# Performance work log

Hardware: AMD Instinct MI355X
Metric: run time of the kernel (lower is better)

## Reference

```python
import jax, jax.numpy as jnp
import numpy as np

BN_EPS = 1e-5


def _gru(x, Wih, Whh, bih, bhh):
    # x: [B,S,D]; Wih: [3H,D]; Whh: [3H,H]; PyTorch gate order (r, z, n)
    B, S, D = x.shape
    H = Whh.shape[1]
    xg = jnp.einsum('bsd,gd->bsg', x, Wih) + bih  # [B,S,3H] precomputed input gates

    def step(h, xg_t):
        hg = h @ Whh.T + bhh
        xr, xz, xn = jnp.split(xg_t, 3, axis=-1)
        hr, hz, hn = jnp.split(hg, 3, axis=-1)
        r = jax.nn.sigmoid(xr + hr)
        z = jax.nn.sigmoid(xz + hz)
        n = jnp.tanh(xn + r * hn)
        h_new = (1.0 - z) * n + z * h
        return h_new, h_new

    h0 = jnp.zeros((B, H), x.dtype)
    _, hs = jax.lax.scan(step, h0, jnp.swapaxes(xg, 0, 1))  # [S,B,H]
    return jnp.swapaxes(hs, 0, 1)


def _lstm(x, Wih, Whh, bih, bhh):
    # x: [B,S,D]; PyTorch gate order (i, f, g, o)
    B, S, D = x.shape
    H = Whh.shape[1]
    xg = jnp.einsum('bsd,gd->bsg', x, Wih) + bih  # [B,S,4H]

    def step(carry, xg_t):
        h, c = carry
        g = xg_t + h @ Whh.T + bhh
        i, f, gg, o = jnp.split(g, 4, axis=-1)
        i = jax.nn.sigmoid(i)
        f = jax.nn.sigmoid(f)
        gg = jnp.tanh(gg)
        o = jax.nn.sigmoid(o)
        c_new = f * c + i * gg
        h_new = o * jnp.tanh(c_new)
        return (h_new, c_new), h_new

    h0 = jnp.zeros((B, H), x.dtype)
    c0 = jnp.zeros((B, H), x.dtype)
    _, hs = jax.lax.scan(step, (h0, c0), jnp.swapaxes(xg, 0, 1))
    return jnp.swapaxes(hs, 0, 1)


def setup_inputs() -> dict:
    key = jax.random.key(0)
    B, S, D, H = 64, 512, 40, 512
    ks = jax.random.split(key, 16)
    s_in = 1.0 / np.sqrt(H)

    def u(k, shape):
        return jax.random.uniform(k, shape, jnp.float32, -s_in, s_in)

    inp = {
        'x': jax.random.normal(ks[0], (B, S, D), jnp.float32),
        # rec1: GRU
        'gru_Wih': u(ks[1], (3 * H, D)),
        'gru_Whh': u(ks[2], (3 * H, H)),
        'gru_bih': u(ks[3], (3 * H,)),
        'gru_bhh': u(ks[4], (3 * H,)),
        # rec2: LSTM over [x, ssr] -> input D+1
        'lstm_Wih': u(ks[5], (4 * H, D + 1)),
        'lstm_Whh': u(ks[6], (4 * H, H)),
        'lstm_bih': u(ks[7], (4 * H,)),
        'lstm_bhh': u(ks[8], (4 * H,)),
        # fc1/fc2/fc3: hidden -> 1
        'fc1_w': u(ks[9], (1, H)), 'fc1_b': u(ks[10], (1,)),
        'fc2_w': u(ks[11], (1, H)), 'fc2_b': u(ks[12], (1,)),
        'fc3_w': u(ks[13], (1, H)), 'fc3_b': u(ks[14], (1,)),
        # BatchNorm1d affine params
        'bn_gamma': jnp.ones((H,), jnp.float32),
        'bn_beta': jnp.zeros((H,), jnp.float32),
    }
    return inp


def reference(x, gru_Wih, gru_Whh, gru_bih, gru_bhh,
              lstm_Wih, lstm_Whh, lstm_bih, lstm_bhh,
              fc1_w, fc1_b, fc2_w, fc2_b, fc3_w, fc3_b,
              bn_gamma, bn_beta):
    B, S, D = x.shape
    o1 = _gru(x, gru_Wih, gru_Whh, gru_bih, gru_bhh)  # [B,S,H]
    # BatchNorm1d (training mode): per-channel stats over (batch, time)
    mean = jnp.mean(o1, axis=(0, 1))
    var = jnp.mean((o1 - mean) ** 2, axis=(0, 1))
    o1 = (o1 - mean) * jax.lax.rsqrt(var + BN_EPS) * bn_gamma + bn_beta
    # gated scalar channel (dropout p=0 is identity)
    sr = jax.nn.relu(o1 @ fc1_w.T + fc1_b)            # [B,S,1]
    w = jnp.abs(jax.nn.sigmoid(o1 @ fc2_w.T + fc2_b))  # [B,S,1]
    ssr = sr * (w + 1.0)                              # [B,S,1]
    x2 = jnp.concatenate([x, ssr], axis=2)            # [B,S,D+1]
    o2 = _lstm(x2, lstm_Wih, lstm_Whh, lstm_bih, lstm_bhh)
    out = jax.nn.relu(o2 @ fc3_w.T + fc3_b)           # [B,S,1]
    return out, ssr
```

## Files before the change

### kernel.cpp

```cpp
#include <hip/hip_runtime.h>
#include <stdint.h>

#define GW 16
#define NU 32
#define HD 512
#define SEQ 512
#define DX 40
#define MB 16

using short8 = __attribute__((ext_vector_type(8))) short;
using f32x4  = __attribute__((ext_vector_type(4))) float;
typedef unsigned long long u64;

__device__ __forceinline__ unsigned short f2bf(float f) {
  uint32_t u = __builtin_bit_cast(uint32_t, f);
  u += 0x7fffu + ((u >> 16) & 1u);
  return (unsigned short)(u >> 16);
}
__device__ __forceinline__ float sigm(float x) { return 1.0f / (1.0f + __expf(-x)); }

#define MFMA_B16(a, b, c) __builtin_amdgcn_mfma_f32_16x16x32_bf16((a), (b), (c), 0, 0, 0)


__global__ __launch_bounds__(640, 1) void gru_kernel(
    const float* __restrict__ x, const float* __restrict__ Wih,
    const float* __restrict__ Whh, const float* __restrict__ bih,
    const float* __restrict__ bhh, unsigned* __restrict__ flags,
    u64* __restrict__ hbuf, float* __restrict__ o1, float* __restrict__ stats)
{
  const int wg = blockIdx.x & (GW - 1);
  const int g  = blockIdx.x >> 4;
  const int tid = threadIdx.x;
  const int wave = tid >> 6;
  const int lane = tid & 63;
  const int u0 = wg * NU;
  const int bg = g * MB;

  __shared__ __align__(16) unsigned short h_s[2][MB][520];
  __shared__ __align__(16) unsigned short x_s[2][MB][72];
  __shared__ float gate_s[3][MB][NU];
  __shared__ float xn_s[MB][NU];
  __shared__ uint32_t h_stage[256];
  __shared__ uint32_t sync_s[4];

  short8 bfrag[18];
  const int myGate = wave >> 1;
  const int ut = wave & 1;
  const int kq = (lane >> 4) * 8;
  if (wave < 6) {
    const int row = myGate * HD + u0 + ut * 16 + (lane & 15);
    for (int kt = 0; kt < 16; ++kt) {
      const float* p = Whh + (size_t)row * HD + kt * 32 + kq;
      short8 f;
#pragma unroll
      for (int j = 0; j < 8; ++j) f[j] = (short)f2bf(p[j]);
      bfrag[kt] = f;
    }
    for (int kt = 16; kt < 18; ++kt) {
      short8 f;
#pragma unroll
      for (int j = 0; j < 8; ++j) {
        int c = kt * 32 + kq + j - HD;
        float v = (myGate < 2 && c < DX) ? Wih[(size_t)row * DX + c] : 0.0f;
        f[j] = (short)f2bf(v);
      }
      bfrag[kt] = f;
    }
  } else if (wave < 8) {
    const int row = 2 * HD + u0 + (wave - 6) * 16 + (lane & 15);
    for (int kt = 0; kt < 2; ++kt) {
      short8 f;
#pragma unroll
      for (int j = 0; j < 8; ++j) {
        int c = kt * 32 + kq + j;
        f[j] = (short)((c < DX) ? f2bf(Wih[(size_t)row * DX + c]) : 0);
      }
      bfrag[kt] = f;
    }
  }

  const int sb = tid >> 5;
  const int su = tid & 31;
  float b_r = 0.f, b_z = 0.f, b_in = 0.f, b_hn = 0.f;
  if (tid < 256) {
    b_r  = bih[u0 + su] + bhh[u0 + su];
    b_z  = bih[HD + u0 + su] + bhh[HD + u0 + su];
    b_in = bih[2 * HD + u0 + su];
    b_hn = bhh[2 * HD + u0 + su];
  }

  for (int i = tid; i < 4160; i += 640) ((u64*)h_s)[i] = 0ull;
  for (int i = tid; i < 576;  i += 640) ((u64*)x_s)[i] = 0ull;
  if (tid < 4) sync_s[tid] = 0;
  __syncthreads();
  {
    int r = tid / 40, c = tid % 40;
    x_s[0][r][c] = f2bf(x[((size_t)(bg + r) * SEQ) * DX + c]);
  }
  __syncthreads();

  unsigned* gf = flags + g * GW * 16;

  if (wave < 8) {
    float hpA = 0.f, hpB = 0.f, ssum = 0.f, ssq = 0.f;
    for (int t = 0; t < SEQ; ++t) {
      if (t) {
        while (__hip_atomic_load(&sync_s[2], __ATOMIC_ACQUIRE,
                                 __HIP_MEMORY_SCOPE_WORKGROUP) < 2u * (unsigned)t)
          __builtin_amdgcn_s_sleep(1);
      }
      const int p = t & 1;
      if (wave < 6) {
        const int m = lane & 15;
        f32x4 a0 = {0.f, 0.f, 0.f, 0.f}, a1 = {0.f, 0.f, 0.f, 0.f};
#pragma unroll
        for (int kt = 0; kt < 16; kt += 2) {
          short8 ha0 = *(const short8*)(&h_s[p][m][kt * 32 + kq]);
          short8 ha1 = *(const short8*)(&h_s[p][m][(kt + 1) * 32 + kq]);
          a0 = MFMA_B16(ha0, bfrag[kt], a0);
          a1 = MFMA_B16(ha1, bfrag[kt + 1], a1);
        }
        short8 ax0 = *(const short8*)(&x_s[p][m][kq]);
        short8 ax1 = *(const short8*)(&x_s[p][m][32 + kq]);
        a0 = MFMA_B16(ax0, bfrag[16], a0);
        a1 = MFMA_B16(ax1, bfrag[17], a1);
        f32x4 acc = a0 + a1;
#pragma unroll
        for (int r = 0; r < 4; ++r)
          gate_s[myGate][(lane >> 4) * 4 + r][ut * 16 + (lane & 15)] = acc[r];
      } else {
        const int m = lane & 15;
        f32x4 acc = {0.f, 0.f, 0.f, 0.f};
        short8 ax0 = *(const short8*)(&x_s[p][m][kq]);
        short8 ax1 = *(const short8*)(&x_s[p][m][32 + kq]);
        acc = MFMA_B16(ax0, bfrag[0], acc);
        acc = MFMA_B16(ax1, bfrag[1], acc);
#pragma unroll
        for (int r = 0; r < 4; ++r)
          xn_s[(lane >> 4) * 4 + r][(wave - 6) * 16 + (lane & 15)] = acc[r];
      }
      asm volatile("s_waitcnt lgkmcnt(0)" ::: "memory");
      if (lane == 0)
        __hip_atomic_fetch_add(&sync_s[0], 1u, __ATOMIC_RELAXED,
                               __HIP_MEMORY_SCOPE_WORKGROUP);
      if (tid < 256) {
        while (__hip_atomic_load(&sync_s[0], __ATOMIC_ACQUIRE,
                                 __HIP_MEMORY_SCOPE_WORKGROUP) < 8u * (unsigned)(t + 1))
          __builtin_amdgcn_s_sleep(1);
        float rA = sigm(gate_s[0][sb][su] + b_r);
        float zA = sigm(gate_s[1][sb][su] + b_z);
        float nA = tanhf(xn_s[sb][su] + b_in + rA * (gate_s[2][sb][su] + b_hn));
        float hA = (1.0f - zA) * nA + zA * hpA;
        float rB = sigm(gate_s[0][sb + 8][su] + b_r);
        float zB = sigm(gate_s[1][sb + 8][su] + b_z);
        float nB = tanhf(xn_s[sb + 8][su] + b_in + rB * (gate_s[2][sb + 8][su] + b_hn));
        float hB = (1.0f - zB) * nB + zB * hpB;
        hpA = hA; hpB = hB;
        ssum += hA + hB; ssq += hA * hA + hB * hB;
        o1[((size_t)(bg + sb) * SEQ + t) * HD + u0 + su] = hA;
        o1[((size_t)(bg + sb + 8) * SEQ + t) * HD + u0 + su] = hB;
        float pA = __shfl_xor(hA, 1);
        float pB = __shfl_xor(hB, 1);
        if ((su & 1) == 0) {
          h_stage[sb * 16 + (su >> 1)] =
              (uint32_t)f2bf(hA) | ((uint32_t)f2bf(pA) << 16);
          h_stage[(sb + 8) * 16 + (su >> 1)] =
              (uint32_t)f2bf(hB) | ((uint32_t)f2bf(pB) << 16);
        }
        asm volatile("s_waitcnt lgkmcnt(0)" ::: "memory");
        if (lane == 0)
          __hip_atomic_fetch_add(&sync_s[1], 1u, __ATOMIC_RELAXED,
                                 __HIP_MEMORY_SCOPE_WORKGROUP);
      }
    }
    if (tid < 256) {
      atomicAdd(&stats[u0 + su], ssum);
      atomicAdd(&stats[HD + u0 + su], ssq);
    }
  } else {
    const int ct = tid - 512;
    const int prow = ct >> 3;
    const int pquad = ct & 7;
    unsigned* myFlag = gf + prow * 16;
    for (int u = 0; u < SEQ - 1; ++u) {
      while (__hip_atomic_load(&sync_s[1], __ATOMIC_ACQUIRE,
                               __HIP_MEMORY_SCOPE_WORKGROUP) < 4u * (unsigned)(u + 1))
        __builtin_amdgcn_s_sleep(1);
      uint32_t w0 = h_stage[prow * 16 + pquad * 2];
      uint32_t w1 = h_stage[prow * 16 + pquad * 2 + 1];
      u64 pub = ((u64)w1 << 32) | (u64)w0;
      u64* hb = hbuf + ((size_t)g * 2 + ((u + 1) & 1)) * 2048;
      __hip_atomic_store(hb + prow * 128 + wg * 8 + pquad, pub,
                         __ATOMIC_RELAXED, __HIP_MEMORY_SCOPE_AGENT);
      asm volatile("s_waitcnt vmcnt(0)" ::: "memory");
      if (lane == 0)
        __hip_atomic_fetch_add(&sync_s[3], 1u, __ATOMIC_RELAXED,
                               __HIP_MEMORY_SCOPE_WORKGROUP);
      if (wave == 8) {
        while (__hip_atomic_load(&sync_s[3], __ATOMIC_ACQUIRE,
                                 __HIP_MEMORY_SCOPE_WORKGROUP) < 2u * (unsigned)(u + 1))
          __builtin_amdgcn_s_sleep(1);
        if (lane == 0)
          __hip_atomic_store(gf + wg * 16, (unsigned)(u + 1),
                             __ATOMIC_RELAXED, __HIP_MEMORY_SCOPE_AGENT);
      }
      float xv[5];
      const int xi = ct * 5;
#pragma unroll
      for (int i = 0; i < 5; ++i) {
        int idx = xi + i, r = idx / 40, c = idx % 40;
        xv[i] = x[((size_t)(bg + r) * SEQ + (u + 1)) * DX + c];
      }
      while (__hip_atomic_load(myFlag, __ATOMIC_RELAXED,
                               __HIP_MEMORY_SCOPE_AGENT) < (unsigned)(u + 1))
        __builtin_amdgcn_s_sleep(1);
      u64 hv[16];
#pragma unroll
      for (int i = 0; i < 16; ++i)
        hv[i] = __hip_atomic_load(hb + i * 128 + ct, __ATOMIC_RELAXED,
                                  __HIP_MEMORY_SCOPE_AGENT);
      const int np = (u + 1) & 1;
#pragma unroll
      for (int i = 0; i < 16; ++i)
        *(u64*)(&h_s[np][i][ct * 4]) = hv[i];
#pragma unroll
      for (int i = 0; i < 5; ++i) {
        int idx = xi + i, r = idx / 40, c = idx % 40;
        x_s[np][r][c] = f2bf(xv[i]);
      }
      asm volatile("s_waitcnt lgkmcnt(0)" ::: "memory");
      if (lane == 0)
        __hip_atomic_fetch_add(&sync_s[2], 1u, __ATOMIC_RELAXED,
                               __HIP_MEMORY_SCOPE_WORKGROUP);
    }
  }
}

__global__ __launch_bounds__(640, 1) void lstm_kernel(
    const float* __restrict__ x, const float* __restrict__ Wih,
    const float* __restrict__ Whh, const float* __restrict__ bih,
    const float* __restrict__ bhh, const float* __restrict__ ssr,
    unsigned* __restrict__ flags, u64* __restrict__ hbuf,
    float* __restrict__ o2)
{
  const int wg = blockIdx.x & (GW - 1);
  const int g  = blockIdx.x >> 4;
  const int tid = threadIdx.x;
  const int wave = tid >> 6;
  const int lane = tid & 63;
  const int u0 = wg * NU;
  const int bg = g * MB;

  __shared__ __align__(16) unsigned short h_s[2][MB][520];
  __shared__ __align__(16) unsigned short x_s[2][MB][72];
  __shared__ float gate_s[4][MB][NU];
  __shared__ uint32_t h_stage[256];
  __shared__ uint32_t sync_s[4];

  short8 bfrag[18];
  const int myGate = wave >> 1;
  const int ut = wave & 1;
  const int kq = (lane >> 4) * 8;
  if (wave < 8) {
    const int row = myGate * HD + u0 + ut * 16 + (lane & 15);
    for (int kt = 0; kt < 16; ++kt) {
      const float* p = Whh + (size_t)row * HD + kt * 32 + kq;
      short8 f;
#pragma unroll
      for (int j = 0; j < 8; ++j) f[j] = (short)f2bf(p[j]);
      bfrag[kt] = f;
    }
    for (int kt = 16; kt < 18; ++kt) {
      short8 f;
#pragma unroll
      for (int j = 0; j < 8; ++j) {
        int c = kt * 32 + kq + j - HD;
        float v = (c < 41) ? Wih[(size_t)row * 41 + c] : 0.0f;
        f[j] = (short)f2bf(v);
      }
      bfrag[kt] = f;
    }
  }

  const int sb = tid >> 5;
  const int su = tid & 31;
  float b_i = 0.f, b_f = 0.f, b_g = 0.f, b_o = 0.f;
  if (tid < 256) {
    b_i = bih[u0 + su] + bhh[u0 + su];
    b_f = bih[HD + u0 + su] + bhh[HD + u0 + su];
    b_g = bih[2 * HD + u0 + su] + bhh[2 * HD + u0 + su];
    b_o = bih[3 * HD + u0 + su] + bhh[3 * HD + u0 + su];
  }

  for (int i = tid; i < 4160; i += 640) ((u64*)h_s)[i] = 0ull;
  for (int i = tid; i < 576;  i += 640) ((u64*)x_s)[i] = 0ull;
  if (tid < 4) sync_s[tid] = 0;
  __syncthreads();
  {
    int r = tid / 40, c = tid % 40;
    x_s[0][r][c] = f2bf(x[((size_t)(bg + r) * SEQ) * DX + c]);
  }
  if (tid < 16) x_s[0][tid][40] = f2bf(ssr[(size_t)(bg + tid) * SEQ]);
  __syncthreads();

  unsigned* gf = flags + g * GW * 16;

  if (wave < 8) {
    float cA = 0.f, cB = 0.f;
    for (int t = 0; t < SEQ; ++t) {
      if (t) {
        while (__hip_atomic_load(&sync_s[2], __ATOMIC_ACQUIRE,
                                 __HIP_MEMORY_SCOPE_WORKGROUP) < 2u * (unsigned)t)
          __builtin_amdgcn_s_sleep(1);
      }
      const int p = t & 1;
      {
        const int m = lane & 15;
        f32x4 a0 = {0.f, 0.f, 0.f, 0.f}, a1 = {0.f, 0.f, 0.f, 0.f};
#pragma unroll
        for (int kt = 0; kt < 16; kt += 2) {
          short8 ha0 = *(const short8*)(&h_s[p][m][kt * 32 + kq]);
          short8 ha1 = *(const short8*)(&h_s[p][m][(kt + 1) * 32 + kq]);
          a0 = MFMA_B16(ha0, bfrag[kt], a0);
          a1 = MFMA_B16(ha1, bfrag[kt + 1], a1);
        }
        short8 ax0 = *(const short8*)(&x_s[p][m][kq]);
        short8 ax1 = *(const short8*)(&x_s[p][m][32 + kq]);
        a0 = MFMA_B16(ax0, bfrag[16], a0);
        a1 = MFMA_B16(ax1, bfrag[17], a1);
        f32x4 acc = a0 + a1;
#pragma unroll
        for (int r = 0; r < 4; ++r)
          gate_s[myGate][(lane >> 4) * 4 + r][ut * 16 + (lane & 15)] = acc[r];
      }
      asm volatile("s_waitcnt lgkmcnt(0)" ::: "memory");
      if (lane == 0)
        __hip_atomic_fetch_add(&sync_s[0], 1u, __ATOMIC_RELAXED,
                               __HIP_MEMORY_SCOPE_WORKGROUP);
      if (tid < 256) {
        while (__hip_atomic_load(&sync_s[0], __ATOMIC_ACQUIRE,
                                 __HIP_MEMORY_SCOPE_WORKGROUP) < 8u * (unsigned)(t + 1))
          __builtin_amdgcn_s_sleep(1);
        float giA = sigm(gate_s[0][sb][su] + b_i);
        float gfA = sigm(gate_s[1][sb][su] + b_f);
        float ggA = tanhf(gate_s[2][sb][su] + b_g);
        float goA = sigm(gate_s[3][sb][su] + b_o);
        cA = gfA * cA + giA * ggA;
        float hA = goA * tanhf(cA);
        float giB = sigm(gate_s[0][sb + 8][su] + b_i);
        float gfB = sigm(gate_s[1][sb + 8][su] + b_f);
        float ggB = tanhf(gate_s[2][sb + 8][su] + b_g);
        float goB = sigm(gate_s[3][sb + 8][su] + b_o);
        cB = gfB * cB + giB * ggB;
        float hB = goB * tanhf(cB);
        o2[((size_t)(bg + sb) * SEQ + t) * HD + u0 + su] = hA;
        o2[((size_t)(bg + sb + 8) * SEQ + t) * HD + u0 + su] = hB;
        float pA = __shfl_xor(hA, 1);
        float pB = __shfl_xor(hB, 1);
        if ((su & 1) == 0) {
          h_stage[sb * 16 + (su >> 1)] =
              (uint32_t)f2bf(hA) | ((uint32_t)f2bf(pA) << 16);
          h_stage[(sb + 8) * 16 + (su >> 1)] =
              (uint32_t)f2bf(hB) | ((uint32_t)f2bf(pB) << 16);
        }
        asm volatile("s_waitcnt lgkmcnt(0)" ::: "memory");
        if (lane == 0)
          __hip_atomic_fetch_add(&sync_s[1], 1u, __ATOMIC_RELAXED,
                                 __HIP_MEMORY_SCOPE_WORKGROUP);
      }
    }
  } else {
    const int ct = tid - 512;
    const int prow = ct >> 3;
    const int pquad = ct & 7;
    unsigned* myFlag = gf + prow * 16;
    for (int u = 0; u < SEQ - 1; ++u) {
      while (__hip_atomic_load(&sync_s[1], __ATOMIC_ACQUIRE,
                               __HIP_MEMORY_SCOPE_WORKGROUP) < 4u * (unsigned)(u + 1))
        __builtin_amdgcn_s_sleep(1);
      uint32_t w0 = h_stage[prow * 16 + pquad * 2];
      uint32_t w1 = h_stage[prow * 16 + pquad * 2 + 1];
      u64 pub = ((u64)w1 << 32) | (u64)w0;
      u64* hb = hbuf + ((size_t)g * 2 + ((u + 1) & 1)) * 2048;
      __hip_atomic_store(hb + prow * 128 + wg * 8 + pquad, pub,
                         __ATOMIC_RELAXED, __HIP_MEMORY_SCOPE_AGENT);
      asm volatile("s_waitcnt vmcnt(0)" ::: "memory");
      if (lane == 0)
        __hip_atomic_fetch_add(&sync_s[3], 1u, __ATOMIC_RELAXED,
                               __HIP_MEMORY_SCOPE_WORKGROUP);
      if (wave == 8) {
        while (__hip_atomic_load(&sync_s[3], __ATOMIC_ACQUIRE,
                                 __HIP_MEMORY_SCOPE_WORKGROUP) < 2u * (unsigned)(u + 1))
          __builtin_amdgcn_s_sleep(1);
        if (lane == 0)
          __hip_atomic_store(gf + wg * 16, (unsigned)(u + 1),
                             __ATOMIC_RELAXED, __HIP_MEMORY_SCOPE_AGENT);
      }
      float xv[5];
      const int xi = ct * 5;
#pragma unroll
      for (int i = 0; i < 5; ++i) {
        int idx = xi + i, r = idx / 40, c = idx % 40;
        xv[i] = x[((size_t)(bg + r) * SEQ + (u + 1)) * DX + c];
      }
      float sv = 0.f;
      if (ct < 16) sv = ssr[(size_t)(bg + ct) * SEQ + (u + 1)];
      while (__hip_atomic_load(myFlag, __ATOMIC_RELAXED,
                               __HIP_MEMORY_SCOPE_AGENT) < (unsigned)(u + 1))
        __builtin_amdgcn_s_sleep(1);
      u64 hv[16];
#pragma unroll
      for (int i = 0; i < 16; ++i)
        hv[i] = __hip_atomic_load(hb + i * 128 + ct, __ATOMIC_RELAXED,
                                  __HIP_MEMORY_SCOPE_AGENT);
      const int np = (u + 1) & 1;
#pragma unroll
      for (int i = 0; i < 16; ++i)
        *(u64*)(&h_s[np][i][ct * 4]) = hv[i];
#pragma unroll
      for (int i = 0; i < 5; ++i) {
        int idx = xi + i, r = idx / 40, c = idx % 40;
        x_s[np][r][c] = f2bf(xv[i]);
      }
      if (ct < 16) x_s[np][ct][40] = f2bf(sv);
      asm volatile("s_waitcnt lgkmcnt(0)" ::: "memory");
      if (lane == 0)
        __hip_atomic_fetch_add(&sync_s[2], 1u, __ATOMIC_RELAXED,
                               __HIP_MEMORY_SCOPE_WORKGROUP);
    }
  }
}

__global__ __launch_bounds__(512) void coef_kernel(
    const float* __restrict__ stats, const float* __restrict__ fc1_w,
    const float* __restrict__ fc1_b, const float* __restrict__ fc2_w,
    const float* __restrict__ fc2_b, const float* __restrict__ gamma,
    const float* __restrict__ beta, float* __restrict__ coef)
{
  __shared__ float r1[512], r2[512];
  const int j = threadIdx.x;
  const float inv_n = 1.0f / 32768.0f;
  float mean = stats[j] * inv_n;
  float var = stats[HD + j] * inv_n - mean * mean;
  float scale = gamma[j] * rsqrtf(var + 1e-5f);
  float shift = beta[j] - mean * scale;
  coef[j] = fc1_w[j] * scale;
  coef[HD + j] = fc2_w[j] * scale;
  r1[j] = fc1_w[j] * shift;
  r2[j] = fc2_w[j] * shift;
  __syncthreads();
  for (int s = 256; s > 0; s >>= 1) {
    if (j < s) { r1[j] += r1[j + s]; r2[j] += r2[j + s]; }
    __syncthreads();
  }
  if (j == 0) {
    coef[2 * HD] = r1[0] + fc1_b[0];
    coef[2 * HD + 1] = r2[0] + fc2_b[0];
  }
}

__global__ __launch_bounds__(256) void ssr_kernel(
    const float* __restrict__ o1, const float* __restrict__ coef,
    float* __restrict__ ssr_ws, float* __restrict__ dssr)
{
  const int row = blockIdx.x * 4 + (threadIdx.x >> 6);
  const int lane = threadIdx.x & 63;
  const float* p = o1 + (size_t)row * HD + lane * 8;
  float s1 = 0.f, s2 = 0.f;
#pragma unroll
  for (int j = 0; j < 8; ++j) {
    float v = p[j];
    s1 += v * coef[lane * 8 + j];
    s2 += v * coef[HD + lane * 8 + j];
  }
#pragma unroll
  for (int off = 32; off > 0; off >>= 1) {
    s1 += __shfl_down(s1, off);
    s2 += __shfl_down(s2, off);
  }
  if (lane == 0) {
    float sr = fmaxf(s1 + coef[2 * HD], 0.0f);
    float w = fabsf(sigm(s2 + coef[2 * HD + 1]));
    float v = sr * (1.0f + w);
    ssr_ws[row] = v;
    dssr[row] = v;
  }
}

__global__ __launch_bounds__(256) void out_kernel(
    const float* __restrict__ o2, const float* __restrict__ fc3_w,
    const float* __restrict__ fc3_b, float* __restrict__ dout)
{
  const int row = blockIdx.x * 4 + (threadIdx.x >> 6);
  const int lane = threadIdx.x & 63;
  const float* p = o2 + (size_t)row * HD + lane * 8;
  float s = 0.f;
#pragma unroll
  for (int j = 0; j < 8; ++j) s += p[j] * fc3_w[lane * 8 + j];
#pragma unroll
  for (int off = 32; off > 0; off >>= 1) s += __shfl_down(s, off);
  if (lane == 0) dout[row] = fmaxf(s + fc3_b[0], 0.0f);
}

extern "C" void kernel_launch(void* const* d_in, const int* in_sizes, int n_in,
                              void* d_out, int out_size, void* d_ws, size_t ws_size,
                              hipStream_t stream) {
  (void)in_sizes; (void)n_in; (void)out_size; (void)ws_size;
  const float* x    = (const float*)d_in[0];
  const float* gWih = (const float*)d_in[1];
  const float* gWhh = (const float*)d_in[2];
  const float* gbih = (const float*)d_in[3];
  const float* gbhh = (const float*)d_in[4];
  const float* lWih = (const float*)d_in[5];
  const float* lWhh = (const float*)d_in[6];
  const float* lbih = (const float*)d_in[7];
  const float* lbhh = (const float*)d_in[8];
  const float* fc1w = (const float*)d_in[9];
  const float* fc1b = (const float*)d_in[10];
  const float* fc2w = (const float*)d_in[11];
  const float* fc2b = (const float*)d_in[12];
  const float* fc3w = (const float*)d_in[13];
  const float* fc3b = (const float*)d_in[14];
  const float* gam  = (const float*)d_in[15];
  const float* bet  = (const float*)d_in[16];
  float* out = (float*)d_out;

  char* ws = (char*)d_ws;
  unsigned* flags_g = (unsigned*)(ws + 0);
  unsigned* flags_l = (unsigned*)(ws + 4096);
  float* stats      = (float*)(ws + 16384);
  float* coef       = (float*)(ws + 24576);
  float* ssr_ws     = (float*)(ws + 32768);
  u64* hbuf_g       = (u64*)(ws + 262144);
  u64* hbuf_l       = (u64*)(ws + 393216);
  float* o1 = (float*)(ws + 1048576);
  float* o2 = o1 + (size_t)64 * SEQ * HD;

  hipMemsetAsync(ws, 0, 20480, stream);

  gru_kernel<<<dim3(64), dim3(640), 0, stream>>>(x, gWih, gWhh, gbih, gbhh,
                                                 flags_g, hbuf_g, o1, stats);
  coef_kernel<<<dim3(1), dim3(512), 0, stream>>>(stats, fc1w, fc1b, fc2w, fc2b,
                                                 gam, bet, coef);
  ssr_kernel<<<dim3(8192), dim3(256), 0, stream>>>(o1, coef, ssr_ws, out + 32768);
  lstm_kernel<<<dim3(64), dim3(640), 0, stream>>>(x, lWih, lWhh, lbih, lbhh, ssr_ws,
                                                  flags_l, hbuf_l, o2);
  out_kernel<<<dim3(8192), dim3(256), 0, stream>>>(o2, fc3w, fc3b, out);
}
```

Measured before the change: 3.542 ms.

## Replace flag-based cross-block handoff with step-tagged hidden-state words

The GRU and LSTM compute waves now publish each hidden-state pair straight to global memory as a 64-bit word that carries the timestep in its upper half. This removes the LDS staging buffer, the intra-block counter handoff to copy waves, the vmcnt wait and the separate per-workgroup flag store. Consumer waves poll the tagged words themselves and reload only those that are stale. The cost is twice the global traffic per hidden-state word, a larger hbuf workspace that must be zeroed, and polling spread over many addresses instead of one flag.

Result: slower. 6.764 ms (+91.0%).

```diff
diff --git a/kernel.cpp b/kernel.cpp
--- a/kernel.cpp
+++ b/kernel.cpp
@@ -25,8 +25,8 @@
 __global__ __launch_bounds__(640, 1) void gru_kernel(
     const float* __restrict__ x, const float* __restrict__ Wih,
     const float* __restrict__ Whh, const float* __restrict__ bih,
-    const float* __restrict__ bhh, unsigned* __restrict__ flags,
-    u64* __restrict__ hbuf, float* __restrict__ o1, float* __restrict__ stats)
+    const float* __restrict__ bhh, u64* __restrict__ hbuf,
+    float* __restrict__ o1, float* __restrict__ stats)
 {
   const int wg = blockIdx.x & (GW - 1);
   const int g  = blockIdx.x >> 4;
@@ -40,7 +40,6 @@
   __shared__ __align__(16) unsigned short x_s[2][MB][72];
   __shared__ float gate_s[3][MB][NU];
   __shared__ float xn_s[MB][NU];
-  __shared__ uint32_t h_stage[256];
   __shared__ uint32_t sync_s[4];
 
   short8 bfrag[18];
@@ -98,8 +97,6 @@
     x_s[0][r][c] = f2bf(x[((size_t)(bg + r) * SEQ) * DX + c]);
   }
   __syncthreads();
-
-  unsigned* gf = flags + g * GW * 16;
 
   if (wave < 8) {
     float hpA = 0.f, hpB = 0.f, ssum = 0.f, ssq = 0.f;
@@ -157,20 +154,21 @@
         float hB = (1.0f - zB) * nB + zB * hpB;
         hpA = hA; hpB = hB;
         ssum += hA + hB; ssq += hA * hA + hB * hB;
+        float pA = __shfl_xor(hA, 1);
+        float pB = __shfl_xor(hB, 1);
+        if (t < SEQ - 1 && (su & 1) == 0) {
+          u64 tg = ((u64)(unsigned)(t + 1)) << 32;
+          u64 wA = (u64)((uint32_t)f2bf(hA) | ((uint32_t)f2bf(pA) << 16)) | tg;
+          u64 wB = (u64)((uint32_t)f2bf(hB) | ((uint32_t)f2bf(pB) << 16)) | tg;
+          u64* hbo = hbuf + ((size_t)g * 2 + ((t + 1) & 1)) * 4096;
+          const int w = wg * 16 + (su >> 1);
+          __hip_atomic_store(hbo + sb * 256 + w, wA,
+                             __ATOMIC_RELAXED, __HIP_MEMORY_SCOPE_AGENT);
+          __hip_atomic_store(hbo + (sb + 8) * 256 + w, wB,
+                             __ATOMIC_RELAXED, __HIP_MEMORY_SCOPE_AGENT);
+        }
         o1[((size_t)(bg + sb) * SEQ + t) * HD + u0 + su] = hA;
         o1[((size_t)(bg + sb + 8) * SEQ + t) * HD + u0 + su] = hB;
-        float pA = __shfl_xor(hA, 1);
-        float pB = __shfl_xor(hB, 1);
-        if ((su & 1) == 0) {
-          h_stage[sb * 16 + (su >> 1)] =
-              (uint32_t)f2bf(hA) | ((uint32_t)f2bf(pA) << 16);
-          h_stage[(sb + 8) * 16 + (su >> 1)] =
-              (uint32_t)f2bf(hB) | ((uint32_t)f2bf(pB) << 16);
-        }
-        asm volatile("s_waitcnt lgkmcnt(0)" ::: "memory");
-        if (lane == 0)
-          __hip_atomic_fetch_add(&sync_s[1], 1u, __ATOMIC_RELAXED,
-                                 __HIP_MEMORY_SCOPE_WORKGROUP);
       }
     }
     if (tid < 256) {
@@ -179,31 +177,8 @@
     }
   } else {
     const int ct = tid - 512;
-    const int prow = ct >> 3;
-    const int pquad = ct & 7;
-    unsigned* myFlag = gf + prow * 16;
     for (int u = 0; u < SEQ - 1; ++u) {
-      while (__hip_atomic_load(&sync_s[1], __ATOMIC_ACQUIRE,
-                               __HIP_MEMORY_SCOPE_WORKGROUP) < 4u * (unsigned)(u + 1))
-        __builtin_amdgcn_s_sleep(1);
-      uint32_t w0 = h_stage[prow * 16 + pquad * 2];
-      uint32_t w1 = h_stage[prow * 16 + pquad * 2 + 1];
-      u64 pub = ((u64)w1 << 32) | (u64)w0;
-      u64* hb = hbuf + ((size_t)g * 2 + ((u + 1) & 1)) * 2048;
-      __hip_atomic_store(hb + prow * 128 + wg * 8 + pquad, pub,
-                         __ATOMIC_RELAXED, __HIP_MEMORY_SCOPE_AGENT);
-      asm volatile("s_waitcnt vmcnt(0)" ::: "memory");
-      if (lane == 0)
-        __hip_atomic_fetch_add(&sync_s[3], 1u, __ATOMIC_RELAXED,
-                               __HIP_MEMORY_SCOPE_WORKGROUP);
-      if (wave == 8) {
-        while (__hip_atomic_load(&sync_s[3], __ATOMIC_ACQUIRE,
-                                 __HIP_MEMORY_SCOPE_WORKGROUP) < 2u * (unsigned)(u + 1))
-          __builtin_amdgcn_s_sleep(1);
-        if (lane == 0)
-          __hip_atomic_store(gf + wg * 16, (unsigned)(u + 1),
-                             __ATOMIC_RELAXED, __HIP_MEMORY_SCOPE_AGENT);
-      }
+      const u64* hbin = hbuf + ((size_t)g * 2 + ((u + 1) & 1)) * 4096;
       float xv[5];
       const int xi = ct * 5;
 #pragma unroll
@@ -211,18 +186,40 @@
         int idx = xi + i, r = idx / 40, c = idx % 40;
         xv[i] = x[((size_t)(bg + r) * SEQ + (u + 1)) * DX + c];
       }
-      while (__hip_atomic_load(myFlag, __ATOMIC_RELAXED,
-                               __HIP_MEMORY_SCOPE_AGENT) < (unsigned)(u + 1))
+      u64 v0[16], v1[16];
+      const int wa = 2 * ct, wb = 2 * ct + 1;
+#pragma unroll
+      for (int i = 0; i < 16; ++i) {
+        v0[i] = __hip_atomic_load(hbin + i * 256 + wa, __ATOMIC_RELAXED,
+                                  __HIP_MEMORY_SCOPE_AGENT);
+        v1[i] = __hip_atomic_load(hbin + i * 256 + wb, __ATOMIC_RELAXED,
+                                  __HIP_MEMORY_SCOPE_AGENT);
+      }
+      const unsigned tg = (unsigned)(u + 1);
+      for (;;) {
+        uint32_t m0 = 0, m1 = 0;
+#pragma unroll
+        for (int i = 0; i < 16; ++i) {
+          m0 |= ((unsigned)(v0[i] >> 32) != tg) ? (1u << i) : 0u;
+          m1 |= ((unsigned)(v1[i] >> 32) != tg) ? (1u << i) : 0u;
+        }
+        if (!(m0 | m1)) break;
         __builtin_amdgcn_s_sleep(1);
-      u64 hv[16];
+#pragma unroll
+        for (int i = 0; i < 16; ++i) {
+          if (m0 & (1u << i))
+            v0[i] = __hip_atomic_load(hbin + i * 256 + wa, __ATOMIC_RELAXED,
+                                      __HIP_MEMORY_SCOPE_AGENT);
+          if (m1 & (1u << i))
+            v1[i] = __hip_atomic_load(hbin + i * 256 + wb, __ATOMIC_RELAXED,
+                                      __HIP_MEMORY_SCOPE_AGENT);
+        }
+      }
+      const int np = (u + 1) & 1;
 #pragma unroll
       for (int i = 0; i < 16; ++i)
-        hv[i] = __hip_atomic_load(hb + i * 128 + ct, __ATOMIC_RELAXED,
-                                  __HIP_MEMORY_SCOPE_AGENT);
-      const int np = (u + 1) & 1;
-#pragma unroll
-      for (int i = 0; i < 16; ++i)
-        *(u64*)(&h_s[np][i][ct * 4]) = hv[i];
+        *(u64*)(&h_s[np][i][ct * 4]) =
+            (v0[i] & 0xffffffffull) | (v1[i] << 32);
 #pragma unroll
       for (int i = 0; i < 5; ++i) {
         int idx = xi + i, r = idx / 40, c = idx % 40;
@@ -240,8 +237,7 @@
     const float* __restrict__ x, const float* __restrict__ Wih,
     const float* __restrict__ Whh, const float* __restrict__ bih,
     const float* __restrict__ bhh, const float* __restrict__ ssr,
-    unsigned* __restrict__ flags, u64* __restrict__ hbuf,
-    float* __restrict__ o2)
+    u64* __restrict__ hbuf, float* __restrict__ o2)
 {
   const int wg = blockIdx.x & (GW - 1);
   const int g  = blockIdx.x >> 4;
@@ -254,7 +250,6 @@
   __shared__ __align__(16) unsigned short h_s[2][MB][520];
   __shared__ __align__(16) unsigned short x_s[2][MB][72];
   __shared__ float gate_s[4][MB][NU];
-  __shared__ uint32_t h_stage[256];
   __shared__ uint32_t sync_s[4];
 
   short8 bfrag[18];
@@ -302,8 +297,6 @@
   }
   if (tid < 16) x_s[0][tid][40] = f2bf(ssr[(size_t)(bg + tid) * SEQ]);
   __syncthreads();
-
-  unsigned* gf = flags + g * GW * 16;
 
   if (wave < 8) {
     float cA = 0.f, cB = 0.f;
@@ -353,49 +346,27 @@
         float goB = sigm(gate_s[3][sb + 8][su] + b_o);
         cB = gfB * cB + giB * ggB;
         float hB = goB * tanhf(cB);
+        float pA = __shfl_xor(hA, 1);
+        float pB = __shfl_xor(hB, 1);
+        if (t < SEQ - 1 && (su & 1) == 0) {
+          u64 tg = ((u64)(unsigned)(t + 1)) << 32;
+          u64 wA = (u64)((uint32_t)f2bf(hA) | ((uint32_t)f2bf(pA) << 16)) | tg;
+          u64 wB = (u64)((uint32_t)f2bf(hB) | ((uint32_t)f2bf(pB) << 16)) | tg;
+          u64* hbo = hbuf + ((size_t)g * 2 + ((t + 1) & 1)) * 4096;
+          const int w = wg * 16 + (su >> 1);
+          __hip_atomic_store(hbo + sb * 256 + w, wA,
+                             __ATOMIC_RELAXED, __HIP_MEMORY_SCOPE_AGENT);
+          __hip_atomic_store(hbo + (sb + 8) * 256 + w, wB,
+                             __ATOMIC_RELAXED, __HIP_MEMORY_SCOPE_AGENT);
+        }
         o2[((size_t)(bg + sb) * SEQ + t) * HD + u0 + su] = hA;
         o2[((size_t)(bg + sb + 8) * SEQ + t) * HD + u0 + su] = hB;
-        float pA = __shfl_xor(hA, 1);
-        float pB = __shfl_xor(hB, 1);
-        if ((su & 1) == 0) {
-          h_stage[sb * 16 + (su >> 1)] =
-              (uint32_t)f2bf(hA) | ((uint32_t)f2bf(pA) << 16);
-          h_stage[(sb + 8) * 16 + (su >> 1)] =
-              (uint32_t)f2bf(hB) | ((uint32_t)f2bf(pB) << 16);
-        }
-        asm volatile("s_waitcnt lgkmcnt(0)" ::: "memory");
-        if (lane == 0)
-          __hip_atomic_fetch_add(&sync_s[1], 1u, __ATOMIC_RELAXED,
-                                 __HIP_MEMORY_SCOPE_WORKGROUP);
       }
     }
   } else {
     const int ct = tid - 512;
-    const int prow = ct >> 3;
-    const int pquad = ct & 7;
-    unsigned* myFlag = gf + prow * 16;
     for (int u = 0; u < SEQ - 1; ++u) {
-      while (__hip_atomic_load(&sync_s[1], __ATOMIC_ACQUIRE,
-                               __HIP_MEMORY_SCOPE_WORKGROUP) < 4u * (unsigned)(u + 1))
-        __builtin_amdgcn_s_sleep(1);
-      uint32_t w0 = h_stage[prow * 16 + pquad * 2];
-      uint32_t w1 = h_stage[prow * 16 + pquad * 2 + 1];
-      u64 pub = ((u64)w1 << 32) | (u64)w0;
-      u64* hb = hbuf + ((size_t)g * 2 + ((u + 1) & 1)) * 2048;
-      __hip_atomic_store(hb + prow * 128 + wg * 8 + pquad, pub,
-                         __ATOMIC_RELAXED, __HIP_MEMORY_SCOPE_AGENT);
-      asm volatile("s_waitcnt vmcnt(0)" ::: "memory");
-      if (lane == 0)
-        __hip_atomic_fetch_add(&sync_s[3], 1u, __ATOMIC_RELAXED,
-                               __HIP_MEMORY_SCOPE_WORKGROUP);
-      if (wave == 8) {
-        while (__hip_atomic_load(&sync_s[3], __ATOMIC_ACQUIRE,
-                                 __HIP_MEMORY_SCOPE_WORKGROUP) < 2u * (unsigned)(u + 1))
-          __builtin_amdgcn_s_sleep(1);
-        if (lane == 0)
-          __hip_atomic_store(gf + wg * 16, (unsigned)(u + 1),
-                             __ATOMIC_RELAXED, __HIP_MEMORY_SCOPE_AGENT);
-      }
+      const u64* hbin = hbuf + ((size_t)g * 2 + ((u + 1) & 1)) * 4096;
       float xv[5];
       const int xi = ct * 5;
 #pragma unroll
@@ -405,18 +376,40 @@
       }
       float sv = 0.f;
       if (ct < 16) sv = ssr[(size_t)(bg + ct) * SEQ + (u + 1)];
-      while (__hip_atomic_load(myFlag, __ATOMIC_RELAXED,
-                               __HIP_MEMORY_SCOPE_AGENT) < (unsigned)(u + 1))
+      u64 v0[16], v1[16];
+      const int wa = 2 * ct, wb = 2 * ct + 1;
+#pragma unroll
+      for (int i = 0; i < 16; ++i) {
+        v0[i] = __hip_atomic_load(hbin + i * 256 + wa, __ATOMIC_RELAXED,
+                                  __HIP_MEMORY_SCOPE_AGENT);
+        v1[i] = __hip_atomic_load(hbin + i * 256 + wb, __ATOMIC_RELAXED,
+                                  __HIP_MEMORY_SCOPE_AGENT);
+      }
+      const unsigned tg = (unsigned)(u + 1);
+      for (;;) {
+        uint32_t m0 = 0, m1 = 0;
+#pragma unroll
+        for (int i = 0; i < 16; ++i) {
+          m0 |= ((unsigned)(v0[i] >> 32) != tg) ? (1u << i) : 0u;
+          m1 |= ((unsigned)(v1[i] >> 32) != tg) ? (1u << i) : 0u;
+        }
+        if (!(m0 | m1)) break;
         __builtin_amdgcn_s_sleep(1);
-      u64 hv[16];
+#pragma unroll
+        for (int i = 0; i < 16; ++i) {
+          if (m0 & (1u << i))
+            v0[i] = __hip_atomic_load(hbin + i * 256 + wa, __ATOMIC_RELAXED,
+                                      __HIP_MEMORY_SCOPE_AGENT);
+          if (m1 & (1u << i))
+            v1[i] = __hip_atomic_load(hbin + i * 256 + wb, __ATOMIC_RELAXED,
+                                      __HIP_MEMORY_SCOPE_AGENT);
+        }
+      }
+      const int np = (u + 1) & 1;
 #pragma unroll
       for (int i = 0; i < 16; ++i)
-        hv[i] = __hip_atomic_load(hb + i * 128 + ct, __ATOMIC_RELAXED,
-                                  __HIP_MEMORY_SCOPE_AGENT);
-      const int np = (u + 1) & 1;
-#pragma unroll
-      for (int i = 0; i < 16; ++i)
-        *(u64*)(&h_s[np][i][ct * 4]) = hv[i];
+        *(u64*)(&h_s[np][i][ct * 4]) =
+            (v0[i] & 0xffffffffull) | (v1[i] << 32);
 #pragma unroll
       for (int i = 0; i < 5; ++i) {
         int idx = xi + i, r = idx / 40, c = idx % 40;
@@ -526,24 +519,23 @@
   float* out = (float*)d_out;
 
   char* ws = (char*)d_ws;
-  unsigned* flags_g = (unsigned*)(ws + 0);
-  unsigned* flags_l = (unsigned*)(ws + 4096);
   float* stats      = (float*)(ws + 16384);
   float* coef       = (float*)(ws + 24576);
   float* ssr_ws     = (float*)(ws + 32768);
   u64* hbuf_g       = (u64*)(ws + 262144);
-  u64* hbuf_l       = (u64*)(ws + 393216);
+  u64* hbuf_l       = (u64*)(ws + 524288);
   float* o1 = (float*)(ws + 1048576);
   float* o2 = o1 + (size_t)64 * SEQ * HD;
 
-  hipMemsetAsync(ws, 0, 20480, stream);
+  hipMemsetAsync(ws + 16384, 0, 4096, stream);
+  hipMemsetAsync(ws + 262144, 0, 524288, stream);
 
   gru_kernel<<<dim3(64), dim3(640), 0, stream>>>(x, gWih, gWhh, gbih, gbhh,
-                                                 flags_g, hbuf_g, o1, stats);
+                                                 hbuf_g, o1, stats);
   coef_kernel<<<dim3(1), dim3(512), 0, stream>>>(stats, fc1w, fc1b, fc2w, fc2b,
                                                  gam, bet, coef);
   ssr_kernel<<<dim3(8192), dim3(256), 0, stream>>>(o1, coef, ssr_ws, out + 32768);
   lstm_kernel<<<dim3(64), dim3(640), 0, stream>>>(x, lWih, lWhh, lbih, lbhh, ssr_ws,
-                                                  flags_l, hbuf_l, o2);
+                                                  hbuf_l, o2);
   out_kernel<<<dim3(8192), dim3(256), 0, stream>>>(o2, fc3w, fc3b, out);
 }
```
